# Kernel tuning notes

Measured on AMD Instinct MI355X. Metric: run time of the kernel, lower is better.

Reference implementation:

```python
import jax, jax.numpy as jnp
import numpy as np

CHANNELS = 256
C8 = CHANNELS // 8


def setup_inputs() -> dict:
    key = jax.random.key(0)
    ks = jax.random.split(key, 7)
    b, c, h, w = 4, CHANNELS, 64, 64
    x = jax.random.normal(ks[0], (b, c, h, w), dtype=jnp.float32)
    # 1x1 conv weights stored as [out_ch, in_ch] (kernel is 1x1)
    s = 1.0 / np.sqrt(c)
    wq = jax.random.uniform(ks[1], (C8, c), jnp.float32, -s, s)
    bq = jax.random.uniform(ks[2], (C8,), jnp.float32, -s, s)
    wk = jax.random.uniform(ks[3], (C8, c), jnp.float32, -s, s)
    bk = jax.random.uniform(ks[4], (C8,), jnp.float32, -s, s)
    wv = jax.random.uniform(ks[5], (c, c), jnp.float32, -s, s)
    bv = jax.random.uniform(ks[6], (c,), jnp.float32, -s, s)
    return {"x": x, "wq": wq, "bq": bq, "wk": wk, "bk": bk, "wv": wv, "bv": bv}


def reference(x, wq, bq, wk, bk, wv, bv):
    b, c, h, w = x.shape
    n = h * w
    xf = x.reshape(b, c, n)                                  # (b, c, n)
    q = jnp.einsum('oc,bcn->bon', wq, xf) + bq[None, :, None]  # (b, c/8, n)
    k = jnp.einsum('oc,bcn->bon', wk, xf) + bk[None, :, None]  # (b, c/8, n)
    v = jnp.einsum('oc,bcn->bon', wv, xf) + bv[None, :, None]  # (b, c, n)
    # attention[b, i, j] = softmax_j( q[:, :, i] . k[:, :, j] )
    scores = jnp.einsum('bdi,bdj->bij', q, k)                # (b, n, n)
    attn = jax.nn.softmax(scores, axis=-1)
    # out = value @ attention^T  -> out[b, c, i] = sum_j v[b, c, j] * attn[b, i, j]
    out = jnp.einsum('bcj,bij->bci', v, attn)                # (b, c, n)
    return out.reshape(b, c, h, w) + x
```

## Files before the change

### kernel.cpp

```cpp
#include <hip/hip_runtime.h>
#include <hip/hip_bf16.h>
#include <stdint.h>

#define CH 256
#define D8 32
#define NN 4096

typedef __attribute__((ext_vector_type(8))) short short8;
typedef __attribute__((ext_vector_type(4))) short s16x4;
typedef __attribute__((ext_vector_type(4))) float f32x4;

#define MFMA16(a,b,c) __builtin_amdgcn_mfma_f32_16x16x32_bf16(a,b,c,0,0,0)

static __device__ __forceinline__ short f2bf(float f) {
  union { float f; uint32_t u; } v; v.f = f;
  uint32_t r = v.u + 0x7fffu + ((v.u >> 16) & 1u);
  return (short)(r >> 16);
}
static __device__ __forceinline__ float bf2f(short h) {
  union { float f; uint32_t u; } v; v.u = ((uint32_t)(uint16_t)h) << 16;
  return v.f;
}
static __device__ __forceinline__ int f2i(float f) {
  union { float f; int i; } v; v.f = f; return v.i;
}
static __device__ __forceinline__ float i2f(int i) {
  union { float f; int i; } v; v.i = i; return v.f;
}

#define DPP_MAX16(V) do { \
    V = fmaxf(V, i2f(__builtin_amdgcn_update_dpp(0, f2i(V), 0xB1, 0xf, 0xf, true)));  \
    V = fmaxf(V, i2f(__builtin_amdgcn_update_dpp(0, f2i(V), 0x4E, 0xf, 0xf, true)));  \
    V = fmaxf(V, i2f(__builtin_amdgcn_update_dpp(0, f2i(V), 0x124, 0xf, 0xf, true))); \
    V = fmaxf(V, i2f(__builtin_amdgcn_update_dpp(0, f2i(V), 0x128, 0xf, 0xf, true))); \
  } while (0)
#define DPP_SUM16(V) do { \
    V += i2f(__builtin_amdgcn_update_dpp(0, f2i(V), 0xB1, 0xf, 0xf, true));  \
    V += i2f(__builtin_amdgcn_update_dpp(0, f2i(V), 0x4E, 0xf, 0xf, true));  \
    V += i2f(__builtin_amdgcn_update_dpp(0, f2i(V), 0x124, 0xf, 0xf, true)); \
    V += i2f(__builtin_amdgcn_update_dpp(0, f2i(V), 0x128, 0xf, 0xf, true)); \
  } while (0)

__global__ __launch_bounds__(256) void prep_kernel(
    const float* __restrict__ x,
    const float* __restrict__ wq, const float* __restrict__ bq,
    const float* __restrict__ wk, const float* __restrict__ bk,
    const float* __restrict__ wv, const float* __restrict__ bv,
    short* __restrict__ xT, short* __restrict__ WQb,
    short* __restrict__ WKb, short* __restrict__ WVb,
    float* __restrict__ BQ, float* __restrict__ BK, float* __restrict__ BV)
{
  int blk = blockIdx.x, t = threadIdx.x;
  if (blk >= 1024) {
    int idx = (blk - 1024) * 256 + t;
    const float LOG2E = 1.4426950408889634f;
    for (int i = idx; i < D8 * CH; i += 2048) WQb[i] = f2bf(wq[i] * LOG2E);
    for (int i = idx; i < D8 * CH; i += 2048) WKb[i] = f2bf(wk[i]);
    for (int i = idx; i < CH * CH; i += 2048) WVb[i] = f2bf(wv[i]);
    if (idx < D8) { BQ[idx] = bq[idx] * LOG2E; BK[idx] = bk[idx]; }
    if (idx < CH) BV[idx] = bv[idx];
    return;
  }
  int b = blk >> 8, ct = (blk >> 6) & 3, nt = blk & 63;
  __shared__ short T[64][65];
  int j = t & 63, i0 = t >> 6;
  const float* xb = x + ((size_t)b * CH + ct * 64) * NN + nt * 64;
  #pragma unroll
  for (int k = 0; k < 16; ++k) {
    int i = k * 4 + i0;
    T[i][j] = f2bf(xb[(size_t)i * NN + j]);
  }
  __syncthreads();
  short* xTb = xT + ((size_t)b * NN + nt * 64) * CH + ct * 64;
  #pragma unroll
  for (int k = 0; k < 16; ++k) {
    int n = k * 4 + i0;
    xTb[(size_t)n * CH + j] = T[j][n];
  }
}

__global__ __launch_bounds__(256) void proj_kernel(
    const short* __restrict__ xT,
    const short* __restrict__ WQb, const short* __restrict__ WKb,
    const short* __restrict__ WVb,
    const float* __restrict__ BQ, const float* __restrict__ BK,
    const float* __restrict__ BV,
    short* __restrict__ Qh, short* __restrict__ Ql,
    short* __restrict__ Kh, short* __restrict__ Kl,
    short* __restrict__ Vo)
{
  int blk = blockIdx.x, t = threadIdx.x;
  int b = blk >> 8, pt = blk & 255;
  int w = t >> 6, lane = t & 63, g = lane >> 4, lr = lane & 15;
  int p0 = pt * 16;
  __shared__ short Vt[4][16][20];

  const short* xrow = xT + ((size_t)b * NN + p0 + lr) * CH + g * 8;
  short8 a[8];
  #pragma unroll
  for (int s = 0; s < 8; ++s) a[s] = *(const short8*)(xrow + s * 32);

  const f32x4 zf = {0.f, 0.f, 0.f, 0.f};

#define WLOAD(DST, TT) do { \
    const short* _W; int _tl; \
    if ((TT) < 2)      { _W = WQb; _tl = (TT); } \
    else if ((TT) < 4) { _W = WKb; _tl = (TT) - 2; } \
    else               { _W = WVb; _tl = (TT) - 4; } \
    _Pragma("unroll") \
    for (int s = 0; s < 8; ++s) \
      DST[s] = *(const short8*)(_W + (size_t)(_tl * 16 + lr) * CH + s * 32 + g * 8); \
  } while (0)

#define WCOMP(CUR, TT) do { \
    int _tloc; const float* _Bs; \
    if ((TT) < 2)      { _Bs = BQ; _tloc = (TT); } \
    else if ((TT) < 4) { _Bs = BK; _tloc = (TT) - 2; } \
    else               { _Bs = BV; _tloc = (TT) - 4; } \
    f32x4 acc = zf; \
    _Pragma("unroll") \
    for (int s = 0; s < 8; ++s) acc = MFMA16(a[s], CUR[s], acc); \
    int o = _tloc * 16 + lr; \
    float bias = _Bs[o]; \
    if ((TT) < 4) { \
      short* Oh = ((TT) < 2) ? Qh : Kh; \
      short* Ol = ((TT) < 2) ? Ql : Kl; \
      _Pragma("unroll") \
      for (int r = 0; r < 4; ++r) { \
        int pos = p0 + g * 4 + r; \
        float val = acc[r] + bias; \
        short hi = f2bf(val); \
        Oh[((size_t)b * NN + pos) * D8 + o] = hi; \
        Ol[((size_t)b * NN + pos) * D8 + o] = f2bf(val - bf2f(hi)); \
      } \
    } else { \
      _Pragma("unroll") \
      for (int r = 0; r < 4; ++r) \
        Vt[w][lr][g * 4 + r] = f2bf(acc[r] + bias); \
      int row = lane >> 2, c4 = (lane & 3) * 4; \
      s16x4 vv = *(const s16x4*)&Vt[w][row][c4]; \
      *(s16x4*)(Vo + ((size_t)b * CH + _tloc * 16 + row) * NN + p0 + c4) = vv; \
    } \
  } while (0)

  int t0 = w * 5;
  short8 bA[8], bB[8];
  WLOAD(bA, t0);
  WLOAD(bB, t0 + 1); WCOMP(bA, t0);
  WLOAD(bA, t0 + 2); WCOMP(bB, t0 + 1);
  WLOAD(bB, t0 + 3); WCOMP(bA, t0 + 2);
  WLOAD(bA, t0 + 4); WCOMP(bB, t0 + 3);
  WCOMP(bA, t0 + 4);
#undef WLOAD
#undef WCOMP
}

__global__ __launch_bounds__(512) void attn_kernel(
    const short* __restrict__ Qh, const short* __restrict__ Ql,
    const short* __restrict__ Kh, const short* __restrict__ Kl,
    const short* __restrict__ V, const float* __restrict__ x,
    float* __restrict__ out)
{
  int blk = blockIdx.x, t = threadIdx.x;
  int xcd = blk & 7, idx = blk >> 3;
  int b = xcd >> 1;
  int qt = ((xcd & 1) << 5) + idx;
  int q0 = qt * 64;
  int w = t >> 6, lane = t & 63, g = lane >> 4, lr = lane & 15;
  int wS = w & 3;
  bool isS = (w < 4);
  int cw0 = wS * 64;

  union Smem {
    struct {
      short P[2][64 * 64];
      float scale[2][64];
      int   flags[2][4];
    } lp;
    float O[CH][67];
  };
  __shared__ Smem sm;
  __shared__ float l_lds[64];

  const short* Qhb = Qh + (size_t)b * NN * D8;
  const short* Qlb = Ql + (size_t)b * NN * D8;
  const short* Khb = Kh + (size_t)b * NN * D8;
  const short* Klb = Kl + (size_t)b * NN * D8;
  const short* Vb = V + (size_t)b * CH * NN;

  short8 aqh, aql;
  if (isS) {
    aqh = *(const short8*)(Qhb + (size_t)(q0 + wS * 16 + lr) * D8 + g * 8);
    aql = *(const short8*)(Qlb + (size_t)(q0 + wS * 16 + lr) * D8 + g * 8);
  }

  const f32x4 zf = {0.f, 0.f, 0.f, 0.f};
  f32x4 O[4][4];
  #pragma unroll
  for (int i = 0; i < 4; ++i)
    #pragma unroll
    for (int j = 0; j < 4; ++j) O[i][j] = zf;
  float m[4] = {-INFINITY, -INFINITY, -INFINITY, -INFINITY};
  float l[4] = {0.f, 0.f, 0.f, 0.f};

  char* Pbase0 = (char*)&sm.lp.P[0][0];
  char* Pbase1 = (char*)&sm.lp.P[1][0];

#define LOADK(KH, KL, KIDX) do { \
    int _k0 = (KIDX) * 64; \
    _Pragma("unroll") \
    for (int _nt = 0; _nt < 4; ++_nt) { \
      size_t _off = (size_t)(_k0 + _nt * 16 + lr) * D8 + g * 8; \
      KH[_nt] = *(const short8*)(Khb + _off); \
      KL[_nt] = *(const short8*)(Klb + _off); \
    } \
  } while (0)

#define SSTEP(KB, KH, KL, NKH, NKL, PBASE, PAR) do { \
    f32x4 S[4]; \
    _Pragma("unroll") \
    for (int nt = 0; nt < 4; ++nt) { \
      f32x4 s_ = MFMA16(aql, KH[nt], zf); \
      s_ = MFMA16(aqh, KL[nt], s_); \
      s_ = MFMA16(aqh, KH[nt], s_); \
      S[nt] = s_; \
    } \
    LOADK(NKH, NKL, ((KB) + 1) & 63); \
    float sc[4]; \
    bool upd = false; \
    _Pragma("unroll") \
    for (int r = 0; r < 4; ++r) { \
      float v = fmaxf(fmaxf(S[0][r], S[1][r]), fmaxf(S[2][r], S[3][r])); \
      DPP_MAX16(v); \
      bool u = v > m[r] + 8.0f;                   \
      upd |= u; \
      float mn = u ? v : m[r]; \
      sc[r] = __builtin_amdgcn_exp2f(m[r] - mn); \
      m[r] = mn; \
    } \
    bool anyupd = __any((int)upd); \
    short pb[4][4]; \
    float rsum[4]; \
    _Pragma("unroll") \
    for (int r = 0; r < 4; ++r) { \
      float acc = 0.f; \
      _Pragma("unroll") \
      for (int nt = 0; nt < 4; ++nt) { \
        float p = __builtin_amdgcn_exp2f(S[nt][r] - m[r]); \
        acc += p; \
        pb[nt][r] = f2bf(p); \
      } \
      rsum[r] = acc; \
    } \
    _Pragma("unroll") \
    for (int r = 0; r < 4; ++r) { \
      float v = rsum[r]; \
      DPP_SUM16(v); \
      l[r] = l[r] * sc[r] + v; \
    } \
    _Pragma("unroll") \
    for (int nt = 0; nt < 4; ++nt) \
      _Pragma("unroll") \
      for (int r = 0; r < 4; ++r) { \
        int qloc = wS * 16 + g * 4 + r; \
        int kk = nt * 16 + lr; \
        int off = (qloc * 128 + kk * 2) ^ ((qloc & 7) << 4); \
        *(short*)((PBASE) + off) = pb[nt][r]; \
      } \
    if (lr == 0) { \
      _Pragma("unroll") \
      for (int r = 0; r < 4; ++r) \
        sm.lp.scale[PAR][wS * 16 + g * 4 + r] = sc[r]; \
    } \
    if (lane == 0) sm.lp.flags[PAR][wS] = anyupd ? 1 : 0; \
  } while (0)

#define PSTEP(CPREV, PBASE, PAR) do { \
    short8 vv[8]; \
    int _k0 = (CPREV) * 64; \
    _Pragma("unroll") \
    for (int _ss = 0; _ss < 2; ++_ss) \
      _Pragma("unroll") \
      for (int _ci = 0; _ci < 4; ++_ci) \
        vv[_ss * 4 + _ci] = *(const short8*)(Vb + \
            (size_t)(cw0 + _ci * 16 + lr) * NN + _k0 + _ss * 32 + g * 8); \
    int need = sm.lp.flags[PAR][0] | sm.lp.flags[PAR][1] | \
               sm.lp.flags[PAR][2] | sm.lp.flags[PAR][3]; \
    if (need) { \
      _Pragma("unroll") \
      for (int mi = 0; mi < 4; ++mi) \
        _Pragma("unroll") \
        for (int r = 0; r < 4; ++r) { \
          float s = sm.lp.scale[PAR][mi * 16 + g * 4 + r]; \
          _Pragma("unroll") \
          for (int ci = 0; ci < 4; ++ci) O[mi][ci][r] *= s; \
        } \
    } \
    __builtin_amdgcn_s_setprio(1); \
    _Pragma("unroll") \
    for (int ss = 0; ss < 2; ++ss) { \
      short8 ap[4]; \
      _Pragma("unroll") \
      for (int mi = 0; mi < 4; ++mi) { \
        int row = mi * 16 + lr; \
        int off = (row * 128 + (ss * 32 + g * 8) * 2) ^ ((row & 7) << 4); \
        ap[mi] = *(const short8*)((PBASE) + off); \
      } \
      _Pragma("unroll") \
      for (int ci = 0; ci < 4; ++ci) { \
        _Pragma("unroll") \
        for (int mi = 0; mi < 4; ++mi) \
          O[mi][ci] = MFMA16(ap[mi], vv[ss * 4 + ci], O[mi][ci]); \
      } \
    } \
    __builtin_amdgcn_s_setprio(0); \
  } while (0)

  short8 khA[4], klA[4], khB[4], klB[4];
  if (isS) LOADK(khA, klA, 0);
  #pragma unroll 1
  for (int kb2 = 0; kb2 < 32; ++kb2) {
    int ke = 2 * kb2;
    if (isS)            SSTEP(ke, khA, klA, khB, klB, Pbase0, 0);
    else if (ke > 0)    PSTEP(ke - 1, Pbase1, 1);
    __syncthreads();
    if (isS)            SSTEP(ke + 1, khB, klB, khA, klA, Pbase1, 1);
    else                PSTEP(ke, Pbase0, 0);
    __syncthreads();
  }
#undef SSTEP
#undef LOADK

  if (isS) {
    if (lr == 0) {
      #pragma unroll
      for (int r = 0; r < 4; ++r)
        l_lds[wS * 16 + g * 4 + r] = l[r];
    }
  } else {
    PSTEP(63, Pbase1, 1);
  }
#undef PSTEP
  __syncthreads();
  if (!isS) {
    #pragma unroll
    for (int mi = 0; mi < 4; ++mi)
      #pragma unroll
      for (int ci = 0; ci < 4; ++ci) {
        int ch = cw0 + ci * 16 + lr;
        #pragma unroll
        for (int r = 0; r < 4; ++r)
          sm.O[ch][mi * 16 + g * 4 + r] = O[mi][ci][r];
      }
  }
  __syncthreads();
  int q = t & 63, crow = t >> 6;
  float linv = 1.0f / l_lds[q];
  const float* xb = x + (size_t)b * CH * NN + q0 + q;
  float* ob = out + (size_t)b * CH * NN + q0 + q;
  #pragma unroll
  for (int oi = 0; oi < 32; ++oi) {
    int ch = crow * 32 + oi;
    ob[(size_t)ch * NN] = sm.O[ch][q] * linv + xb[(size_t)ch * NN];
  }
}

extern "C" void kernel_launch(void* const* d_in, const int* in_sizes, int n_in,
                              void* d_out, int out_size, void* d_ws, size_t ws_size,
                              hipStream_t stream) {
  const float* x  = (const float*)d_in[0];
  const float* wq = (const float*)d_in[1];
  const float* bq = (const float*)d_in[2];
  const float* wk = (const float*)d_in[3];
  const float* bk = (const float*)d_in[4];
  const float* wv = (const float*)d_in[5];
  const float* bv = (const float*)d_in[6];
  char* ws = (char*)d_ws;
  short* xT  = (short*)(ws);
  short* Qh  = (short*)(ws + 8388608);
  short* Ql  = (short*)(ws + 9437184);
  short* Kh  = (short*)(ws + 10485760);
  short* Kl  = (short*)(ws + 11534336);
  short* Vo  = (short*)(ws + 12582912);
  short* WQb = (short*)(ws + 20971520);
  short* WKb = (short*)(ws + 20987904);
  short* WVb = (short*)(ws + 21004288);
  float* BQ  = (float*)(ws + 21135360);
  float* BK  = (float*)(ws + 21135488);
  float* BV  = (float*)(ws + 21135616);

  prep_kernel<<<1032, 256, 0, stream>>>(x, wq, bq, wk, bk, wv, bv,
                                        xT, WQb, WKb, WVb, BQ, BK, BV);
  proj_kernel<<<1024, 256, 0, stream>>>(xT, WQb, WKb, WVb, BQ, BK, BV,
                                        Qh, Ql, Kh, Kl, Vo);
  attn_kernel<<<256, 512, 0, stream>>>(Qh, Ql, Kh, Kl, Vo, x, (float*)d_out);
}
```

Baseline: 229.1 us.

## Fuse x transpose into projection and deepen K/V prefetch in attention

The separate transpose-to-bf16 pass over x is removed. The projection kernel now loads fp32 x tiles directly, converts them and transposes them through LDS, which avoids writing and rereading an 8 MB intermediate. In the attention kernel, K and V tiles are prefetched two steps ahead into dedicated register buffers, and V loads move out of the P-step critical path. __syncthreads is replaced with an explicit lgkmcnt wait plus s_barrier so that outstanding global loads are not drained at each barrier. The trade-off is higher register pressure and strided fp32 loads in the projection kernel.

```diff
diff --git a/kernel.cpp b/kernel.cpp
--- a/kernel.cpp
+++ b/kernel.cpp
@@ -11,6 +11,7 @@
 typedef __attribute__((ext_vector_type(4))) float f32x4;
 
 #define MFMA16(a,b,c) __builtin_amdgcn_mfma_f32_16x16x32_bf16(a,b,c,0,0,0)
+#define BAR() asm volatile("s_waitcnt lgkmcnt(0)\n\ts_barrier" ::: "memory")
 
 static __device__ __forceinline__ short f2bf(float f) {
   union { float f; uint32_t u; } v; v.f = f;
@@ -41,46 +42,24 @@
     V += i2f(__builtin_amdgcn_update_dpp(0, f2i(V), 0x128, 0xf, 0xf, true)); \
   } while (0)
 
-__global__ __launch_bounds__(256) void prep_kernel(
-    const float* __restrict__ x,
+__global__ __launch_bounds__(256) void prep_w(
     const float* __restrict__ wq, const float* __restrict__ bq,
     const float* __restrict__ wk, const float* __restrict__ bk,
     const float* __restrict__ wv, const float* __restrict__ bv,
-    short* __restrict__ xT, short* __restrict__ WQb,
-    short* __restrict__ WKb, short* __restrict__ WVb,
+    short* __restrict__ WQb, short* __restrict__ WKb, short* __restrict__ WVb,
     float* __restrict__ BQ, float* __restrict__ BK, float* __restrict__ BV)
 {
-  int blk = blockIdx.x, t = threadIdx.x;
-  if (blk >= 1024) {
-    int idx = (blk - 1024) * 256 + t;
-    const float LOG2E = 1.4426950408889634f;
-    for (int i = idx; i < D8 * CH; i += 2048) WQb[i] = f2bf(wq[i] * LOG2E);
-    for (int i = idx; i < D8 * CH; i += 2048) WKb[i] = f2bf(wk[i]);
-    for (int i = idx; i < CH * CH; i += 2048) WVb[i] = f2bf(wv[i]);
-    if (idx < D8) { BQ[idx] = bq[idx] * LOG2E; BK[idx] = bk[idx]; }
-    if (idx < CH) BV[idx] = bv[idx];
-    return;
-  }
-  int b = blk >> 8, ct = (blk >> 6) & 3, nt = blk & 63;
-  __shared__ short T[64][65];
-  int j = t & 63, i0 = t >> 6;
-  const float* xb = x + ((size_t)b * CH + ct * 64) * NN + nt * 64;
-  #pragma unroll
-  for (int k = 0; k < 16; ++k) {
-    int i = k * 4 + i0;
-    T[i][j] = f2bf(xb[(size_t)i * NN + j]);
-  }
-  __syncthreads();
-  short* xTb = xT + ((size_t)b * NN + nt * 64) * CH + ct * 64;
-  #pragma unroll
-  for (int k = 0; k < 16; ++k) {
-    int n = k * 4 + i0;
-    xTb[(size_t)n * CH + j] = T[j][n];
-  }
+  int idx = blockIdx.x * 256 + threadIdx.x;
+  const float LOG2E = 1.4426950408889634f;
+  for (int i = idx; i < D8 * CH; i += 2048) WQb[i] = f2bf(wq[i] * LOG2E);
+  for (int i = idx; i < D8 * CH; i += 2048) WKb[i] = f2bf(wk[i]);
+  for (int i = idx; i < CH * CH; i += 2048) WVb[i] = f2bf(wv[i]);
+  if (idx < D8) { BQ[idx] = bq[idx] * LOG2E; BK[idx] = bk[idx]; }
+  if (idx < CH) BV[idx] = bv[idx];
 }
 
 __global__ __launch_bounds__(256) void proj_kernel(
-    const short* __restrict__ xT,
+    const float* __restrict__ x,
     const short* __restrict__ WQb, const short* __restrict__ WKb,
     const short* __restrict__ WVb,
     const float* __restrict__ BQ, const float* __restrict__ BK,
@@ -93,12 +72,26 @@
   int b = blk >> 8, pt = blk & 255;
   int w = t >> 6, lane = t & 63, g = lane >> 4, lr = lane & 15;
   int p0 = pt * 16;
+  __shared__ short xls[16][264];
   __shared__ short Vt[4][16][20];
 
-  const short* xrow = xT + ((size_t)b * NN + p0 + lr) * CH + g * 8;
+  {
+    int c0 = t >> 2, pj = (t & 3) * 4;
+    #pragma unroll
+    for (int pass = 0; pass < 4; ++pass) {
+      int c = c0 + pass * 64;
+      float4 v = *(const float4*)(x + ((size_t)b * CH + c) * NN + p0 + pj);
+      xls[pj + 0][c] = f2bf(v.x);
+      xls[pj + 1][c] = f2bf(v.y);
+      xls[pj + 2][c] = f2bf(v.z);
+      xls[pj + 3][c] = f2bf(v.w);
+    }
+  }
+  __syncthreads();
+
   short8 a[8];
   #pragma unroll
-  for (int s = 0; s < 8; ++s) a[s] = *(const short8*)(xrow + s * 32);
+  for (int s = 0; s < 8; ++s) a[s] = *(const short8*)&xls[lr][s * 32 + g * 8];
 
   const f32x4 zf = {0.f, 0.f, 0.f, 0.f};
 
@@ -207,7 +200,7 @@
   char* Pbase1 = (char*)&sm.lp.P[1][0];
 
 #define LOADK(KH, KL, KIDX) do { \
-    int _k0 = (KIDX) * 64; \
+    int _k0 = ((KIDX) & 63) * 64; \
     _Pragma("unroll") \
     for (int _nt = 0; _nt < 4; ++_nt) { \
       size_t _off = (size_t)(_k0 + _nt * 16 + lr) * D8 + g * 8; \
@@ -216,7 +209,17 @@
     } \
   } while (0)
 
-#define SSTEP(KB, KH, KL, NKH, NKL, PBASE, PAR) do { \
+#define LOADV(VV, KIDX) do { \
+    int _k0 = ((KIDX) & 63) * 64; \
+    _Pragma("unroll") \
+    for (int _ss = 0; _ss < 2; ++_ss) \
+      _Pragma("unroll") \
+      for (int _ci = 0; _ci < 4; ++_ci) \
+        VV[_ss * 4 + _ci] = *(const short8*)(Vb + \
+            (size_t)(cw0 + _ci * 16 + lr) * NN + _k0 + _ss * 32 + g * 8); \
+  } while (0)
+
+#define SSTEP(KB, KH, KL, PBASE, PAR) do { \
     f32x4 S[4]; \
     _Pragma("unroll") \
     for (int nt = 0; nt < 4; ++nt) { \
@@ -225,7 +228,7 @@
       s_ = MFMA16(aqh, KH[nt], s_); \
       S[nt] = s_; \
     } \
-    LOADK(NKH, NKL, ((KB) + 1) & 63); \
+    LOADK(KH, KL, (KB) + 2); \
     float sc[4]; \
     bool upd = false; \
     _Pragma("unroll") \
@@ -275,15 +278,7 @@
     if (lane == 0) sm.lp.flags[PAR][wS] = anyupd ? 1 : 0; \
   } while (0)
 
-#define PSTEP(CPREV, PBASE, PAR) do { \
-    short8 vv[8]; \
-    int _k0 = (CPREV) * 64; \
-    _Pragma("unroll") \
-    for (int _ss = 0; _ss < 2; ++_ss) \
-      _Pragma("unroll") \
-      for (int _ci = 0; _ci < 4; ++_ci) \
-        vv[_ss * 4 + _ci] = *(const short8*)(Vb + \
-            (size_t)(cw0 + _ci * 16 + lr) * NN + _k0 + _ss * 32 + g * 8); \
+#define PSTEP(CPREV, PBASE, PAR, VV) do { \
     int need = sm.lp.flags[PAR][0] | sm.lp.flags[PAR][1] | \
                sm.lp.flags[PAR][2] | sm.lp.flags[PAR][3]; \
     if (need) { \
@@ -310,23 +305,25 @@
       for (int ci = 0; ci < 4; ++ci) { \
         _Pragma("unroll") \
         for (int mi = 0; mi < 4; ++mi) \
-          O[mi][ci] = MFMA16(ap[mi], vv[ss * 4 + ci], O[mi][ci]); \
+          O[mi][ci] = MFMA16(ap[mi], VV[ss * 4 + ci], O[mi][ci]); \
       } \
     } \
     __builtin_amdgcn_s_setprio(0); \
-  } while (0)
-
-  short8 khA[4], klA[4], khB[4], klB[4];
-  if (isS) LOADK(khA, klA, 0);
+    LOADV(VV, (CPREV) + 2); \
+  } while (0)
+
+  short8 khA[4], klA[4], khB[4], klB[4], vA[8], vB[8];
+  if (isS) { LOADK(khA, klA, 0); LOADK(khB, klB, 1); }
+  else     { LOADV(vA, 0); LOADV(vB, 1); }
   #pragma unroll 1
   for (int kb2 = 0; kb2 < 32; ++kb2) {
     int ke = 2 * kb2;
-    if (isS)            SSTEP(ke, khA, klA, khB, klB, Pbase0, 0);
-    else if (ke > 0)    PSTEP(ke - 1, Pbase1, 1);
-    __syncthreads();
-    if (isS)            SSTEP(ke + 1, khB, klB, khA, klA, Pbase1, 1);
-    else                PSTEP(ke, Pbase0, 0);
-    __syncthreads();
+    if (isS)         SSTEP(ke, khA, klA, Pbase0, 0);
+    else if (ke > 0) PSTEP(ke - 1, Pbase1, 1, vB);
+    BAR();
+    if (isS) SSTEP(ke + 1, khB, klB, Pbase1, 1);
+    else     PSTEP(ke, Pbase0, 0, vA);
+    BAR();
   }
 #undef SSTEP
 #undef LOADK
@@ -338,9 +335,10 @@
         l_lds[wS * 16 + g * 4 + r] = l[r];
     }
   } else {
-    PSTEP(63, Pbase1, 1);
+    PSTEP(63, Pbase1, 1, vB);
   }
 #undef PSTEP
+#undef LOADV
   __syncthreads();
   if (!isS) {
     #pragma unroll
@@ -376,22 +374,21 @@
   const float* wv = (const float*)d_in[5];
   const float* bv = (const float*)d_in[6];
   char* ws = (char*)d_ws;
-  short* xT  = (short*)(ws);
-  short* Qh  = (short*)(ws + 8388608);
-  short* Ql  = (short*)(ws + 9437184);
-  short* Kh  = (short*)(ws + 10485760);
-  short* Kl  = (short*)(ws + 11534336);
-  short* Vo  = (short*)(ws + 12582912);
-  short* WQb = (short*)(ws + 20971520);
-  short* WKb = (short*)(ws + 20987904);
-  short* WVb = (short*)(ws + 21004288);
-  float* BQ  = (float*)(ws + 21135360);
-  float* BK  = (float*)(ws + 21135488);
-  float* BV  = (float*)(ws + 21135616);
-
-  prep_kernel<<<1032, 256, 0, stream>>>(x, wq, bq, wk, bk, wv, bv,
-                                        xT, WQb, WKb, WVb, BQ, BK, BV);
-  proj_kernel<<<1024, 256, 0, stream>>>(xT, WQb, WKb, WVb, BQ, BK, BV,
+  short* Qh  = (short*)(ws);
+  short* Ql  = (short*)(ws + 1048576);
+  short* Kh  = (short*)(ws + 2097152);
+  short* Kl  = (short*)(ws + 3145728);
+  short* Vo  = (short*)(ws + 4194304);
+  short* WQb = (short*)(ws + 12582912);
+  short* WKb = (short*)(ws + 12599296);
+  short* WVb = (short*)(ws + 12615680);
+  float* BQ  = (float*)(ws + 12746752);
+  float* BK  = (float*)(ws + 12746880);
+  float* BV  = (float*)(ws + 12747008);
+
+  prep_w<<<8, 256, 0, stream>>>(wq, bq, wk, bk, wv, bv,
+                                WQb, WKb, WVb, BQ, BK, BV);
+  proj_kernel<<<1024, 256, 0, stream>>>(x, WQb, WKb, WVb, BQ, BK, BV,
                                         Qh, Ql, Kh, Kl, Vo);
   attn_kernel<<<256, 512, 0, stream>>>(Qh, Ql, Kh, Kl, Vo, x, (float*)d_out);
 }
```

Result: slower. 298.5 us (+30.3%).
